# Kernel optimization log

Measured on AMD Instinct MI355X. Metric: run time of the kernel, lower is better.

Reference implementation:

```python
import jax, jax.numpy as jnp
import numpy as np

B, T, C = 8, 1024, 2048
N_HEAD = 16
HEAD = C // N_HEAD  # 128


def setup_inputs() -> dict:
    key = jax.random.key(0)
    k1, k2, k3 = jax.random.split(key, 3)
    scale = 0.02
    x = jax.random.normal(k1, (B, T, C), dtype=jnp.float32)
    W_attn = jax.random.normal(k2, (C, 3 * C), dtype=jnp.float32) * scale
    b_attn = jnp.zeros((3 * C,), dtype=jnp.float32)
    W_proj = jax.random.normal(k3, (C, C), dtype=jnp.float32) * scale
    b_proj = jnp.zeros((C,), dtype=jnp.float32)
    return {"x": x, "W_attn": W_attn, "b_attn": b_attn, "W_proj": W_proj, "b_proj": b_proj}


def reference(x, W_attn, b_attn, W_proj, b_proj):
    Bq, Tq, Cq = x.shape
    qkv = x @ W_attn + b_attn                       # [B,T,3C]
    q, k, v = jnp.split(qkv, 3, axis=2)             # each [B,T,C]
    def heads(t):
        return t.reshape(Bq, Tq, N_HEAD, HEAD).transpose(0, 2, 1, 3)  # [B,H,T,D]
    q, k, v = heads(q), heads(k), heads(v)
    scores = jnp.einsum('bhqd,bhkd->bhqk', q, k) / jnp.sqrt(jnp.float32(HEAD))
    causal = jnp.tril(jnp.ones((Tq, Tq), dtype=bool))
    scores = jnp.where(causal, scores, jnp.float32(-1e9))
    attn = jax.nn.softmax(scores, axis=-1)          # [B,H,T,T]
    y = jnp.einsum('bhqk,bhkd->bhqd', attn, v)      # [B,H,T,D]
    y = y.transpose(0, 2, 1, 3).reshape(Bq, Tq, Cq) # [B,T,C]
    return y @ W_proj + b_proj
```

## Files before the change

kernel.cpp:

```cpp
#include <hip/hip_runtime.h>
#include <hip/hip_bf16.h>


typedef unsigned short u16;
typedef __bf16 bf16x8 __attribute__((ext_vector_type(8)));
typedef float f32x4 __attribute__((ext_vector_type(4)));

#define B_ 8
#define T_ 1024
#define C_ 2048
#define NH 16
#define HD 128
#define BH (B_*NH)

__device__ __forceinline__ u16 f2b(float f){
  __bf16 h = (__bf16)f; return __builtin_bit_cast(u16, h);
}
__device__ __forceinline__ unsigned pk2(float x, float y){
  return (unsigned)f2b(x) | ((unsigned)f2b(y) << 16);
}
__device__ __forceinline__ bf16x8 ldfrag(const u16* p){
  uint4 u = *(const uint4*)p; return __builtin_bit_cast(bf16x8, u);
}
__device__ __forceinline__ void glds16(const u16* g, const u16* l){
  __builtin_amdgcn_global_load_lds(
      (const __attribute__((address_space(1))) void*)g,
      (__attribute__((address_space(3))) void*)l, 16, 0, 0);
}
__device__ __forceinline__ void sbar(){
  __builtin_amdgcn_sched_barrier(0);
  __builtin_amdgcn_s_barrier();
  __builtin_amdgcn_sched_barrier(0);
}

__global__ __launch_bounds__(256) void cvt_bf16(
    const float4* __restrict__ in, ushort4* __restrict__ outp, int n4)
{
  int i = blockIdx.x*256 + threadIdx.x;
  const int stride = gridDim.x*256;
  for (; i < n4; i += stride){
    float4 f = in[i];
    ushort4 o; o.x = f2b(f.x); o.y = f2b(f.y); o.z = f2b(f.z); o.w = f2b(f.w);
    outp[i] = o;
  }
}

__global__ __launch_bounds__(256) void transpose_cvt(
    const float* __restrict__ in, u16* __restrict__ outp, int R, int C)
{
  __shared__ u16 tile[64][65];
  const int t = threadIdx.x;
  const int r0 = blockIdx.y * 64, c0 = blockIdx.x * 64;
#pragma unroll
  for (int ii = 0; ii < 16; ++ii){
    int idx = t + ii*256; int r = idx >> 6, c = idx & 63;
    tile[r][c] = f2b(in[(size_t)(r0 + r)*C + c0 + c]);
  }
  __syncthreads();
#pragma unroll
  for (int ii = 0; ii < 16; ++ii){
    int idx = t + ii*256; int r = idx >> 6, c = idx & 63;
    outp[(size_t)(c0 + r)*R + r0 + c] = tile[c][r];
  }
}

__device__ __forceinline__ void qkv_epilogue(
    const f32x4 acc[4][4], const float* bias, int bx, int by,
    int wm, int wn, int lq, int ln,
    u16* qb, u16* kb, u16* vb)
{
  const int tensor = bx >> 4, h = bx & 15, b = by >> 3, t0 = (by & 7)*128;
  u16* tb = tensor==0 ? qb : (tensor==1 ? kb : vb);
  u16* op = tb + ((size_t)(b*NH + h)*T_ + t0)*HD;
#pragma unroll
  for (int j=0;j<4;j++){
    const float bv = bias[bx*128 + wn*64 + j*16 + ln];
    const int n = wn*64 + j*16 + ln;
#pragma unroll
    for (int i=0;i<4;i++){
      const int m0 = wm*64 + i*16 + lq*4;
#pragma unroll
      for (int r=0;r<4;r++)
        op[(size_t)(m0 + r)*HD + n] = f2b(acc[i][j][r] + bv);
    }
  }
}

__global__ __launch_bounds__(512,2) void gemm_qkv_8p(
    const u16* __restrict__ Xb, const u16* __restrict__ Wt,
    const float* __restrict__ bias,
    u16* __restrict__ qb, u16* __restrict__ kb, u16* __restrict__ vb)
{
  __shared__ u16 lds[2][2][256*64];
  const int t = threadIdx.x;
  const int lane = t & 63, wid = t >> 6;
  const int lq = lane >> 4, ln = lane & 15;
  const int wm = wid >> 2, wn = wid & 3;

  const int bid0 = blockIdx.x;
  const int bid = (bid0 & 7)*96 + (bid0 >> 3);
  const int bx = bid % 24, by = bid / 24;

  const int rl  = (wid << 4) + (lane >> 3);
  const int sw0 = (lane & 7) ^ (rl & 7);
  const int sw1 = (lane & 7) ^ ((rl + 8) & 7);
  const u16* Ag = Xb + ((size_t)(by*256) + rl)*2048;
  const u16* Bg = Wt + ((size_t)(bx*256) + rl)*2048;
  const size_t q0off = (size_t)sw0*8;
  const size_t q1off = (size_t)8*2048 + (size_t)sw1*8;

#define STAGE(buf_, op_, h_, T_) do { \
    const u16* s_ = (op_ ? Bg : Ag) + (size_t)(h_)*(128*2048) + (size_t)(T_)*64; \
    const u16* d_ = &lds[buf_][op_][(((h_)*128) + (wid<<4))*64]; \
    glds16(s_ + q0off, d_); \
    glds16(s_ + q1off, d_ + 8*64); \
  } while(0)

  const int swr0 = (0*4 + lq) ^ (ln & 7);
  const int swr1 = (1*4 + lq) ^ (ln & 7);

  const f32x4 fz = {0.f,0.f,0.f,0.f};
  f32x4 acc[8][4];
#pragma unroll
  for (int f=0;f<8;f++)
#pragma unroll
    for (int g=0;g<4;g++) acc[f][g] = fz;

  STAGE(0,0,0,0); STAGE(0,0,1,0); STAGE(0,1,0,0); STAGE(0,1,1,0);
  STAGE(1,1,0,1); STAGE(1,1,1,1); STAGE(1,0,0,1);
  asm volatile("s_waitcnt vmcnt(6)" ::: "memory");
  sbar();

  for (int T = 0; T < 32; ++T){
    const int b = T & 1;
    const u16* As = lds[b][0];
    const u16* Bs = lds[b][1];
    bf16x8 a0[4][2], a4[4][2], bfr[4][2];

#pragma unroll
    for (int f=0;f<4;f++){
      a0[f][0]  = ldfrag(&As[(wm*128 + f*16 + ln)*64 + swr0*8]);
      a0[f][1]  = ldfrag(&As[(wm*128 + f*16 + ln)*64 + swr1*8]);
      bfr[f][0] = ldfrag(&Bs[(wn*64  + f*16 + ln)*64 + swr0*8]);
      bfr[f][1] = ldfrag(&Bs[(wn*64  + f*16 + ln)*64 + swr1*8]);
    }
    if (T+1 < 32) STAGE(b^1, 0, 1, T+1);
    sbar();
    __builtin_amdgcn_s_setprio(1);
#pragma unroll
    for (int f=0;f<4;f++)
#pragma unroll
      for (int g=0;g<2;g++){
        acc[f][g] = __builtin_amdgcn_mfma_f32_16x16x32_bf16(a0[f][0], bfr[g][0], acc[f][g], 0,0,0);
        acc[f][g] = __builtin_amdgcn_mfma_f32_16x16x32_bf16(a0[f][1], bfr[g][1], acc[f][g], 0,0,0);
      }
    __builtin_amdgcn_s_setprio(0);
    sbar();

#pragma unroll
    for (int f=0;f<4;f++){
      a4[f][0] = ldfrag(&As[(wm*128 + (f+4)*16 + ln)*64 + swr0*8]);
      a4[f][1] = ldfrag(&As[(wm*128 + (f+4)*16 + ln)*64 + swr1*8]);
    }
    if (T+2 < 32) STAGE(b, 1, 0, T+2);
    sbar();
    __builtin_amdgcn_s_setprio(1);
#pragma unroll
    for (int f=0;f<4;f++)
#pragma unroll
      for (int g=0;g<2;g++){
        acc[f+4][g] = __builtin_amdgcn_mfma_f32_16x16x32_bf16(a4[f][0], bfr[g][0], acc[f+4][g], 0,0,0);
        acc[f+4][g] = __builtin_amdgcn_mfma_f32_16x16x32_bf16(a4[f][1], bfr[g][1], acc[f+4][g], 0,0,0);
      }
    __builtin_amdgcn_s_setprio(0);
    sbar();

    if (T+2 < 32) STAGE(b, 1, 1, T+2);
    sbar();
    __builtin_amdgcn_s_setprio(1);
#pragma unroll
    for (int f=0;f<4;f++)
#pragma unroll
      for (int g=2;g<4;g++){
        acc[f+4][g] = __builtin_amdgcn_mfma_f32_16x16x32_bf16(a4[f][0], bfr[g][0], acc[f+4][g], 0,0,0);
        acc[f+4][g] = __builtin_amdgcn_mfma_f32_16x16x32_bf16(a4[f][1], bfr[g][1], acc[f+4][g], 0,0,0);
      }
    __builtin_amdgcn_s_setprio(0);
    sbar();

    if (T+2 < 32) STAGE(b, 0, 0, T+2);
    if (T >= 30) asm volatile("s_waitcnt vmcnt(0)" ::: "memory");
    else         asm volatile("s_waitcnt vmcnt(6)" ::: "memory");
    sbar();
    __builtin_amdgcn_s_setprio(1);
#pragma unroll
    for (int f=0;f<4;f++)
#pragma unroll
      for (int g=2;g<4;g++){
        acc[f][g] = __builtin_amdgcn_mfma_f32_16x16x32_bf16(a0[f][0], bfr[g][0], acc[f][g], 0,0,0);
        acc[f][g] = __builtin_amdgcn_mfma_f32_16x16x32_bf16(a0[f][1], bfr[g][1], acc[f][g], 0,0,0);
      }
    __builtin_amdgcn_s_setprio(0);
    sbar();
  }
#undef STAGE

  const int tensor = bx >> 3;
  u16* tb = tensor==0 ? qb : (tensor==1 ? kb : vb);
  const int m_base = by*256 + wm*128;
#pragma unroll
  for (int g=0; g<4; ++g){
    const int ncol = (bx & 7)*256 + wn*64 + g*16 + ln;
    const float bv = bias[tensor*2048 + ncol];
    const int h = ncol >> 7, d = ncol & 127;
#pragma unroll
    for (int f=0; f<8; ++f){
      const int m0 = m_base + f*16 + lq*4;
      const int bb = m0 >> 10, tt = m0 & 1023;
      u16* op = tb + ((size_t)(bb*NH + h)*T_ + tt)*HD + d;
#pragma unroll
      for (int r=0;r<4;++r)
        op[(size_t)r*HD] = f2b(acc[f][g][r] + bv);
    }
  }
}

__global__ __launch_bounds__(256,2) void gemm_qkv_f32(
    const float* __restrict__ X, const u16* __restrict__ Wt, const float* __restrict__ bias,
    u16* __restrict__ qb, u16* __restrict__ kb, u16* __restrict__ vb)
{
  __shared__ u16 As[128*32];
  __shared__ u16 Bs[128*32];
  const int t = threadIdx.x;
  const int bx = blockIdx.x, by = blockIdx.y;
  const int lane = t & 63, wv = t >> 6;
  const int lq = lane >> 4, ln = lane & 15;
  const int wm = wv >> 1, wn = wv & 1;

  const int ar = t >> 1, ah = t & 1;
  const float* Ap = X + (size_t)(by*128 + ar)*2048 + ah*16;
  u16* AsW = &As[ar*32 + ah*16];

  const int c0 = t, c1 = 256 + t;
  const u16* Bp0 = Wt + (size_t)(bx*128 + (c0 >> 2))*2048 + (c0 & 3)*8;
  const u16* Bp1 = Wt + (size_t)(bx*128 + (c1 >> 2))*2048 + (c1 & 3)*8;
  const u16* BsW0 = &Bs[(wv*64)*8];
  const u16* BsW1 = &Bs[(256 + wv*64)*8];

  const f32x4 fz = {0.f,0.f,0.f,0.f};
  f32x4 acc[4][4];
#pragma unroll
  for (int i=0;i<4;i++)
#pragma unroll
    for (int j=0;j<4;j++) acc[i][j] = fz;

  for (int kt = 0; kt < 64; ++kt){
    float4 a0 = *(const float4*)(Ap);
    float4 a1 = *(const float4*)(Ap + 4);
    float4 a2 = *(const float4*)(Ap + 8);
    float4 a3 = *(const float4*)(Ap + 12);
    Ap += 32;
    __syncthreads();
    uint4 w0, w1;
    w0.x = pk2(a0.x,a0.y); w0.y = pk2(a0.z,a0.w);
    w0.z = pk2(a1.x,a1.y); w0.w = pk2(a1.z,a1.w);
    w1.x = pk2(a2.x,a2.y); w1.y = pk2(a2.z,a2.w);
    w1.z = pk2(a3.x,a3.y); w1.w = pk2(a3.z,a3.w);
    *(uint4*)(AsW) = w0; *(uint4*)(AsW + 8) = w1;
    glds16(Bp0, BsW0);
    glds16(Bp1, BsW1);
    Bp0 += 32; Bp1 += 32;
    __syncthreads();
    bf16x8 af[4], bf[4];
#pragma unroll
    for (int i=0;i<4;i++) af[i] = ldfrag(&As[(wm*64 + i*16 + ln)*32 + lq*8]);
#pragma unroll
    for (int j=0;j<4;j++) bf[j] = ldfrag(&Bs[(wn*64 + j*16 + ln)*32 + lq*8]);
#pragma unroll
    for (int i=0;i<4;i++)
#pragma unroll
      for (int j=0;j<4;j++)
        acc[i][j] = __builtin_amdgcn_mfma_f32_16x16x32_bf16(af[i], bf[j], acc[i][j], 0,0,0);
  }
  qkv_epilogue(acc, bias, bx, by, wm, wn, lq, ln, qb, kb, vb);
}

__global__ __launch_bounds__(256,2) void gemm_proj(
    const u16* __restrict__ Y, const u16* __restrict__ Wt, const float* __restrict__ bias,
    float* __restrict__ outp)
{
  __shared__ u16 As[128*32];
  __shared__ u16 Bs[128*32];
  const int t = threadIdx.x;
  const int bx = blockIdx.x, by = blockIdx.y;
  const int lane = t & 63, wv = t >> 6;
  const int lq = lane >> 4, ln = lane & 15;
  const int wm = wv >> 1, wn = wv & 1;

  const int c0 = t, c1 = 256 + t;
  const int rA0 = by*128 + (c0 >> 2), rA1 = by*128 + (c1 >> 2);
  const u16* Ya0 = Y + ((size_t)((rA0 >> 10)*NH)*T_ + (rA0 & 1023))*HD;
  const u16* Ya1 = Y + ((size_t)((rA1 >> 10)*NH)*T_ + (rA1 & 1023))*HD;
  const int kc0 = (c0 & 3)*8, kc1 = (c1 & 3)*8;
  const u16* AsW0 = &As[(wv*64)*8];
  const u16* AsW1 = &As[(256 + wv*64)*8];

  const u16* Bp0 = Wt + (size_t)(bx*128 + (c0 >> 2))*2048 + (c0 & 3)*8;
  const u16* Bp1 = Wt + (size_t)(bx*128 + (c1 >> 2))*2048 + (c1 & 3)*8;
  const u16* BsW0 = &Bs[(wv*64)*8];
  const u16* BsW1 = &Bs[(256 + wv*64)*8];

  const f32x4 fz = {0.f,0.f,0.f,0.f};
  f32x4 acc[4][4];
#pragma unroll
  for (int i=0;i<4;i++)
#pragma unroll
    for (int j=0;j<4;j++) acc[i][j] = fz;

  for (int kt = 0; kt < 64; ++kt){
    __syncthreads();
    {
      const int k0 = kt*32 + kc0, k1 = kt*32 + kc1;
      glds16(Ya0 + (size_t)(k0 >> 7)*(T_*HD) + (k0 & 127), AsW0);
      glds16(Ya1 + (size_t)(k1 >> 7)*(T_*HD) + (k1 & 127), AsW1);
      glds16(Bp0, BsW0);
      glds16(Bp1, BsW1);
      Bp0 += 32; Bp1 += 32;
    }
    __syncthreads();
    bf16x8 af[4], bf[4];
#pragma unroll
    for (int i=0;i<4;i++) af[i] = ldfrag(&As[(wm*64 + i*16 + ln)*32 + lq*8]);
#pragma unroll
    for (int j=0;j<4;j++) bf[j] = ldfrag(&Bs[(wn*64 + j*16 + ln)*32 + lq*8]);
#pragma unroll
    for (int i=0;i<4;i++)
#pragma unroll
      for (int j=0;j<4;j++)
        acc[i][j] = __builtin_amdgcn_mfma_f32_16x16x32_bf16(af[i], bf[j], acc[i][j], 0,0,0);
  }

  float* op = outp + (size_t)(by*128)*2048 + bx*128;
#pragma unroll
  for (int j=0;j<4;j++){
    const float bv = bias[bx*128 + wn*64 + j*16 + ln];
    const int n = wn*64 + j*16 + ln;
#pragma unroll
    for (int i=0;i<4;i++){
      const int m0 = wm*64 + i*16 + lq*4;
#pragma unroll
      for (int r=0;r<4;r++)
        op[(size_t)(m0 + r)*2048 + n] = acc[i][j][r] + bv;
    }
  }
}

__global__ __launch_bounds__(256,2) void attn_fwd(
    u16* qy, const u16* __restrict__ kk, const u16* __restrict__ vv)
{
  __shared__ u16 Ks[64*128];
  __shared__ u16 Vt[128*64];
  __shared__ u16 Ps[4*32*64];
  const int qt = 7 - blockIdx.x, bh = blockIdx.y;
  const int t = threadIdx.x;
  const int lane = t & 63, wv = t >> 6;
  const int lq = lane >> 4, ln = lane & 15;

  bf16x8 qf[2][4];
#pragma unroll
  for (int i=0;i<2;i++)
#pragma unroll
    for (int kc=0;kc<4;kc++){
      int qrow = qt*128 + wv*32 + i*16 + ln;
      qf[i][kc] = ldfrag(&qy[((size_t)bh*T_ + qrow)*HD + kc*32 + lq*8]);
    }

  const f32x4 fz = {0.f,0.f,0.f,0.f};
  f32x4 o[2][8];
#pragma unroll
  for (int i=0;i<2;i++)
#pragma unroll
    for (int jd=0;jd<8;jd++) o[i][jd] = fz;
  float mi[2][4], li[2][4];
#pragma unroll
  for (int i=0;i<2;i++)
#pragma unroll
    for (int r=0;r<4;r++){ mi[i][r] = -1e30f; li[i][r] = 0.f; }

  const float scale = 0.08838834764831843f;
  const int kr = t & 63, dbase = (t >> 6)*32;
  const int nkt = 2*qt + 2;

  uint4 kreg[4];
  uint4 vreg[4];
  {
    const uint4* ksrc = (const uint4*)(kk + (size_t)bh*T_*HD);
#pragma unroll
    for (int ii=0; ii<4; ++ii) kreg[ii] = ksrc[t + ii*256];
#pragma unroll
    for (int ch=0; ch<4; ++ch)
      vreg[ch] = *(const uint4*)&vv[((size_t)bh*T_ + kr)*HD + dbase + ch*8];
  }

  for (int kt = 0; kt < nkt; ++kt){
    __syncthreads();
    uint4* kdst = (uint4*)Ks;
#pragma unroll
    for (int ii=0; ii<4; ++ii){
      const int c = t + ii*256;
      kdst[(c & ~15) | ((c & 15) ^ ((c >> 4) & 7))] = kreg[ii];
    }
#pragma unroll
    for (int ch=0; ch<4; ++ch){
      const u16* e = (const u16*)&vreg[ch];
#pragma unroll
      for (int j=0; j<8; ++j){
        const int d = dbase + ch*8 + j;
        Vt[d*64 + (kr ^ ((d & 7) << 3))] = e[j];
      }
    }
    __syncthreads();

    {
      const int ktn = (kt+1 < nkt) ? kt+1 : kt;
      const uint4* ksrc = (const uint4*)(kk + ((size_t)bh*T_ + ktn*64)*HD);
#pragma unroll
      for (int ii=0; ii<4; ++ii) kreg[ii] = ksrc[t + ii*256];
#pragma unroll
      for (int ch=0; ch<4; ++ch)
        vreg[ch] = *(const uint4*)&vv[((size_t)bh*T_ + ktn*64 + kr)*HD + dbase + ch*8];
    }

    f32x4 s[2][4];
#pragma unroll
    for (int i=0;i<2;i++)
#pragma unroll
      for (int j=0;j<4;j++) s[i][j] = fz;
    __builtin_amdgcn_s_setprio(1);
#pragma unroll
    for (int j=0;j<4;j++){
      bf16x8 kf[4];
      const int krow = j*16 + ln;
      const int ksw = (krow & 7) << 3;
#pragma unroll
      for (int kc=0;kc<4;kc++)
        kf[kc] = ldfrag(&Ks[krow*128 + ((kc*32 + lq*8) ^ ksw)]);
#pragma unroll
      for (int i=0;i<2;i++)
#pragma unroll
        for (int kc=0;kc<4;kc++)
          s[i][j] = __builtin_amdgcn_mfma_f32_16x16x32_bf16(qf[i][kc], kf[kc], s[i][j], 0,0,0);
    }
    __builtin_amdgcn_s_setprio(0);

#pragma unroll
    for (int i=0;i<2;i++)
#pragma unroll
      for (int j=0;j<4;j++)
#pragma unroll
        for (int r=0;r<4;r++){
          int qg = qt*128 + wv*32 + i*16 + lq*4 + r;
          int kg = kt*64 + j*16 + ln;
          float sv = s[i][j][r]*scale;
          s[i][j][r] = (kg > qg) ? -1e30f : sv;
        }

    float mxv[2][4];
#pragma unroll
    for (int i=0;i<2;i++)
#pragma unroll
      for (int r=0;r<4;r++){
        float mx = fmaxf(fmaxf(s[i][0][r], s[i][1][r]), fmaxf(s[i][2][r], s[i][3][r]));
        mx = fmaxf(mx, __shfl_xor(mx, 1));
        mx = fmaxf(mx, __shfl_xor(mx, 2));
        mx = fmaxf(mx, __shfl_xor(mx, 4));
        mx = fmaxf(mx, __shfl_xor(mx, 8));
        mxv[i][r] = mx;
      }
    bool ok = true;
#pragma unroll
    for (int i=0;i<2;i++)
#pragma unroll
      for (int r=0;r<4;r++) ok = ok && (mxv[i][r] <= mi[i][r] + 8.0f);
    if (!__all((int)ok)){
#pragma unroll
      for (int i=0;i<2;i++)
#pragma unroll
        for (int r=0;r<4;r++){
          float mnew = fmaxf(mi[i][r], mxv[i][r]);
          float alpha = __expf(mi[i][r] - mnew);
          li[i][r] *= alpha;
          mi[i][r] = mnew;
#pragma unroll
          for (int jd=0;jd<8;jd++) o[i][jd][r] *= alpha;
        }
    }
#pragma unroll
    for (int i=0;i<2;i++)
#pragma unroll
      for (int r=0;r<4;r++){
        float rs = 0.f;
#pragma unroll
        for (int j=0;j<4;j++){
          float p = __expf(s[i][j][r] - mi[i][r]);
          s[i][j][r] = p; rs += p;
        }
        rs += __shfl_xor(rs, 1); rs += __shfl_xor(rs, 2);
        rs += __shfl_xor(rs, 4); rs += __shfl_xor(rs, 8);
        li[i][r] += rs;
      }

#pragma unroll
    for (int i=0;i<2;i++)
#pragma unroll
      for (int j=0;j<4;j++)
#pragma unroll
        for (int r=0;r<4;r++){
          const int rr = i*16 + lq*4 + r;
          Ps[wv*2048 + rr*64 + ((j*16 + ln) ^ ((rr & 7) << 3))] = f2b(s[i][j][r]);
        }

    bf16x8 pf[2][2];
#pragma unroll
    for (int i=0;i<2;i++){
      const int prow = i*16 + ln;
      const int psw = (prow & 7) << 3;
#pragma unroll
      for (int kc=0;kc<2;kc++)
        pf[i][kc] = ldfrag(&Ps[wv*2048 + prow*64 + ((kc*32 + lq*8) ^ psw)]);
    }
    __builtin_amdgcn_s_setprio(1);
#pragma unroll
    for (int jd=0;jd<8;jd++){
      const int vrow = jd*16 + ln;
      const int vsw = (vrow & 7) << 3;
#pragma unroll
      for (int kc=0;kc<2;kc++){
        bf16x8 vf = ldfrag(&Vt[vrow*64 + ((kc*32 + lq*8) ^ vsw)]);
#pragma unroll
        for (int i=0;i<2;i++)
          o[i][jd] = __builtin_amdgcn_mfma_f32_16x16x32_bf16(pf[i][kc], vf, o[i][jd], 0,0,0);
      }
    }
    __builtin_amdgcn_s_setprio(0);
  }

#pragma unroll
  for (int i=0;i<2;i++)
#pragma unroll
    for (int r=0;r<4;r++){
      float inv = 1.f / li[i][r];
      int row = qt*128 + wv*32 + i*16 + lq*4 + r;
#pragma unroll
      for (int jd=0;jd<8;jd++)
        qy[((size_t)bh*T_ + row)*HD + jd*16 + ln] = f2b(o[i][jd][r] * inv);
    }
}

extern "C" void kernel_launch(void* const* d_in, const int* in_sizes, int n_in,
                              void* d_out, int out_size, void* d_ws, size_t ws_size,
                              hipStream_t stream)
{
  const float* x      = (const float*)d_in[0];
  const float* W_attn = (const float*)d_in[1];
  const float* b_attn = (const float*)d_in[2];
  const float* W_proj = (const float*)d_in[3];
  const float* b_proj = (const float*)d_in[4];
  float* out = (float*)d_out;

  u16* Wat = (u16*)d_ws;
  u16* Wpt = Wat + (size_t)6144*2048;
  u16* qb  = Wpt + (size_t)2048*2048;
  u16* xb  = qb  + (size_t)BH*T_*HD;
  u16* kb  = (u16*)d_out;
  u16* vb  = kb + (size_t)BH*T_*HD;

  const size_t need = ((size_t)6144*2048 + (size_t)2048*2048
                       + 2*(size_t)BH*T_*HD) * sizeof(u16);

  hipLaunchKernelGGL(transpose_cvt, dim3(96,32,1), dim3(256,1,1), 0, stream,
                     W_attn, Wat, 2048, 6144);
  hipLaunchKernelGGL(transpose_cvt, dim3(32,32,1), dim3(256,1,1), 0, stream,
                     W_proj, Wpt, 2048, 2048);
  if (ws_size >= need){
    hipLaunchKernelGGL(cvt_bf16, dim3(1024,1,1), dim3(256,1,1), 0, stream,
                       (const float4*)x, (ushort4*)xb, (B_*T_*C_)/4);
    hipLaunchKernelGGL(gemm_qkv_8p, dim3(768,1,1), dim3(512,1,1), 0, stream,
                       xb, Wat, b_attn, qb, kb, vb);
  } else {
    hipLaunchKernelGGL(gemm_qkv_f32, dim3(48,64,1), dim3(256,1,1), 0, stream,
                       x, Wat, b_attn, qb, kb, vb);
  }
  hipLaunchKernelGGL(attn_fwd, dim3(8,BH,1), dim3(256,1,1), 0, stream,
                     qb, kb, vb);
  hipLaunchKernelGGL(gemm_proj, dim3(16,64,1), dim3(256,1,1), 0, stream,
                     qb, Wpt, b_proj, out);
}
```

Before: 627.8 us.

## Port projection GEMM to 8-phase pipelined kernel and skip fully-masked attention tiles

Replaces the simple 128x128 projection GEMM with a 256x256-tile, 512-thread, double-buffered, 8-phase pipelined kernel. It reads the head-major attention output directly through a per-row address mapping. In attention, each wave now skips the QK/softmax/PV work for key tiles that lie entirely above its causal diagonal. It also simplifies the QKV swizzle offset (sw1 equals sw0 because rl+8 has the same low 3 bits). The main risks are more register pressure and fewer blocks (256) for the projection, and wave divergence inside the attention block around barriers.

```diff
diff --git a/kernel.cpp b/kernel.cpp
--- a/kernel.cpp
+++ b/kernel.cpp
@@ -103,11 +103,10 @@
 
   const int rl  = (wid << 4) + (lane >> 3);
   const int sw0 = (lane & 7) ^ (rl & 7);
-  const int sw1 = (lane & 7) ^ ((rl + 8) & 7);
   const u16* Ag = Xb + ((size_t)(by*256) + rl)*2048;
   const u16* Bg = Wt + ((size_t)(bx*256) + rl)*2048;
   const size_t q0off = (size_t)sw0*8;
-  const size_t q1off = (size_t)8*2048 + (size_t)sw1*8;
+  const size_t q1off = (size_t)8*2048 + (size_t)sw0*8;
 
 #define STAGE(buf_, op_, h_, T_) do { \
     const u16* s_ = (op_ ? Bg : Ag) + (size_t)(h_)*(128*2048) + (size_t)(T_)*64; \
@@ -221,6 +220,145 @@
 #pragma unroll
       for (int r=0;r<4;++r)
         op[(size_t)r*HD] = f2b(acc[f][g][r] + bv);
+    }
+  }
+}
+
+__global__ __launch_bounds__(512,2) void gemm_proj_8p(
+    const u16* __restrict__ Y, const u16* __restrict__ Wt,
+    const float* __restrict__ bias, float* __restrict__ outp)
+{
+  __shared__ u16 lds[2][2][256*64];
+  const int t = threadIdx.x;
+  const int lane = t & 63, wid = t >> 6;
+  const int lq = lane >> 4, ln = lane & 15;
+  const int wm = wid >> 2, wn = wid & 3;
+
+  const int bid0 = blockIdx.x;
+  const int bid = (bid0 & 7)*32 + (bid0 >> 3);
+  const int bx = bid & 7, by = bid >> 3;
+
+  const int rl  = (wid << 4) + (lane >> 3);
+  const int sw0 = (lane & 7) ^ (rl & 7);
+  const u16* Bg = Wt + ((size_t)(bx*256) + rl)*2048;
+  const size_t bq0 = (size_t)sw0*8;
+  const size_t arow0 = ((size_t)(by >> 2)*16)*1024 + (size_t)(by & 3)*256 + rl;
+
+#define STAGEP(buf_, op_, h_, Tt_) do { \
+    const u16* d_ = &lds[buf_][op_][(((h_)*128) + (wid<<4))*64]; \
+    if (op_){ \
+      const u16* s_ = Bg + (size_t)(h_)*(128*2048) + (size_t)(Tt_)*64; \
+      glds16(s_ + bq0, d_); \
+      glds16(s_ + (size_t)8*2048 + bq0, d_ + 8*64); \
+    } else { \
+      const u16* s_ = Y + (arow0 + (size_t)((Tt_) >> 1)*1024 + (size_t)(h_)*128)*128 \
+                        + ((Tt_) & 1)*64 + sw0*8; \
+      glds16(s_, d_); \
+      glds16(s_ + 8*128, d_ + 8*64); \
+    } \
+  } while(0)
+
+  const int swr0 = (0*4 + lq) ^ (ln & 7);
+  const int swr1 = (1*4 + lq) ^ (ln & 7);
+
+  const f32x4 fz = {0.f,0.f,0.f,0.f};
+  f32x4 acc[8][4];
+#pragma unroll
+  for (int f=0;f<8;f++)
+#pragma unroll
+    for (int g=0;g<4;g++) acc[f][g] = fz;
+
+  STAGEP(0,0,0,0); STAGEP(0,0,1,0); STAGEP(0,1,0,0); STAGEP(0,1,1,0);
+  STAGEP(1,1,0,1); STAGEP(1,1,1,1); STAGEP(1,0,0,1);
+  asm volatile("s_waitcnt vmcnt(6)" ::: "memory");
+  sbar();
+
+  for (int T = 0; T < 32; ++T){
+    const int b = T & 1;
+    const u16* As = lds[b][0];
+    const u16* Bs = lds[b][1];
+    bf16x8 a0[4][2], a4[4][2], bfr[4][2];
+
+#pragma unroll
+    for (int f=0;f<4;f++){
+      a0[f][0]  = ldfrag(&As[(wm*128 + f*16 + ln)*64 + swr0*8]);
+      a0[f][1]  = ldfrag(&As[(wm*128 + f*16 + ln)*64 + swr1*8]);
+      bfr[f][0] = ldfrag(&Bs[(wn*64  + f*16 + ln)*64 + swr0*8]);
+      bfr[f][1] = ldfrag(&Bs[(wn*64  + f*16 + ln)*64 + swr1*8]);
+    }
+    if (T+1 < 32) STAGEP(b^1, 0, 1, T+1);
+    sbar();
+    __builtin_amdgcn_s_setprio(1);
+#pragma unroll
+    for (int f=0;f<4;f++)
+#pragma unroll
+      for (int g=0;g<2;g++){
+        acc[f][g] = __builtin_amdgcn_mfma_f32_16x16x32_bf16(a0[f][0], bfr[g][0], acc[f][g], 0,0,0);
+        acc[f][g] = __builtin_amdgcn_mfma_f32_16x16x32_bf16(a0[f][1], bfr[g][1], acc[f][g], 0,0,0);
+      }
+    __builtin_amdgcn_s_setprio(0);
+    sbar();
+
+#pragma unroll
+    for (int f=0;f<4;f++){
+      a4[f][0] = ldfrag(&As[(wm*128 + (f+4)*16 + ln)*64 + swr0*8]);
+      a4[f][1] = ldfrag(&As[(wm*128 + (f+4)*16 + ln)*64 + swr1*8]);
+    }
+    if (T+2 < 32) STAGEP(b, 1, 0, T+2);
+    sbar();
+    __builtin_amdgcn_s_setprio(1);
+#pragma unroll
+    for (int f=0;f<4;f++)
+#pragma unroll
+      for (int g=0;g<2;g++){
+        acc[f+4][g] = __builtin_amdgcn_mfma_f32_16x16x32_bf16(a4[f][0], bfr[g][0], acc[f+4][g], 0,0,0);
+        acc[f+4][g] = __builtin_amdgcn_mfma_f32_16x16x32_bf16(a4[f][1], bfr[g][1], acc[f+4][g], 0,0,0);
+      }
+    __builtin_amdgcn_s_setprio(0);
+    sbar();
+
+    if (T+2 < 32) STAGEP(b, 1, 1, T+2);
+    sbar();
+    __builtin_amdgcn_s_setprio(1);
+#pragma unroll
+    for (int f=0;f<4;f++)
+#pragma unroll
+      for (int g=2;g<4;g++){
+        acc[f+4][g] = __builtin_amdgcn_mfma_f32_16x16x32_bf16(a4[f][0], bfr[g][0], acc[f+4][g], 0,0,0);
+        acc[f+4][g] = __builtin_amdgcn_mfma_f32_16x16x32_bf16(a4[f][1], bfr[g][1], acc[f+4][g], 0,0,0);
+      }
+    __builtin_amdgcn_s_setprio(0);
+    sbar();
+
+    if (T+2 < 32) STAGEP(b, 0, 0, T+2);
+    if (T >= 30) asm volatile("s_waitcnt vmcnt(0)" ::: "memory");
+    else         asm volatile("s_waitcnt vmcnt(6)" ::: "memory");
+    sbar();
+    __builtin_amdgcn_s_setprio(1);
+#pragma unroll
+    for (int f=0;f<4;f++)
+#pragma unroll
+      for (int g=2;g<4;g++){
+        acc[f][g] = __builtin_amdgcn_mfma_f32_16x16x32_bf16(a0[f][0], bfr[g][0], acc[f][g], 0,0,0);
+        acc[f][g] = __builtin_amdgcn_mfma_f32_16x16x32_bf16(a0[f][1], bfr[g][1], acc[f][g], 0,0,0);
+      }
+    __builtin_amdgcn_s_setprio(0);
+    sbar();
+  }
+#undef STAGEP
+
+  const int m_base = by*256 + wm*128;
+#pragma unroll
+  for (int g=0; g<4; ++g){
+    const int ncol = bx*256 + wn*64 + g*16 + ln;
+    const float bv = bias[ncol];
+#pragma unroll
+    for (int f=0; f<8; ++f){
+      const int m0 = m_base + f*16 + lq*4;
+      float* op = outp + (size_t)m0*2048 + ncol;
+#pragma unroll
+      for (int r=0;r<4;++r)
+        op[(size_t)r*2048] = acc[f][g][r] + bv;
     }
   }
 }
@@ -285,76 +423,6 @@
   qkv_epilogue(acc, bias, bx, by, wm, wn, lq, ln, qb, kb, vb);
 }
 
-__global__ __launch_bounds__(256,2) void gemm_proj(
-    const u16* __restrict__ Y, const u16* __restrict__ Wt, const float* __restrict__ bias,
-    float* __restrict__ outp)
-{
-  __shared__ u16 As[128*32];
-  __shared__ u16 Bs[128*32];
-  const int t = threadIdx.x;
-  const int bx = blockIdx.x, by = blockIdx.y;
-  const int lane = t & 63, wv = t >> 6;
-  const int lq = lane >> 4, ln = lane & 15;
-  const int wm = wv >> 1, wn = wv & 1;
-
-  const int c0 = t, c1 = 256 + t;
-  const int rA0 = by*128 + (c0 >> 2), rA1 = by*128 + (c1 >> 2);
-  const u16* Ya0 = Y + ((size_t)((rA0 >> 10)*NH)*T_ + (rA0 & 1023))*HD;
-  const u16* Ya1 = Y + ((size_t)((rA1 >> 10)*NH)*T_ + (rA1 & 1023))*HD;
-  const int kc0 = (c0 & 3)*8, kc1 = (c1 & 3)*8;
-  const u16* AsW0 = &As[(wv*64)*8];
-  const u16* AsW1 = &As[(256 + wv*64)*8];
-
-  const u16* Bp0 = Wt + (size_t)(bx*128 + (c0 >> 2))*2048 + (c0 & 3)*8;
-  const u16* Bp1 = Wt + (size_t)(bx*128 + (c1 >> 2))*2048 + (c1 & 3)*8;
-  const u16* BsW0 = &Bs[(wv*64)*8];
-  const u16* BsW1 = &Bs[(256 + wv*64)*8];
-
-  const f32x4 fz = {0.f,0.f,0.f,0.f};
-  f32x4 acc[4][4];
-#pragma unroll
-  for (int i=0;i<4;i++)
-#pragma unroll
-    for (int j=0;j<4;j++) acc[i][j] = fz;
-
-  for (int kt = 0; kt < 64; ++kt){
-    __syncthreads();
-    {
-      const int k0 = kt*32 + kc0, k1 = kt*32 + kc1;
-      glds16(Ya0 + (size_t)(k0 >> 7)*(T_*HD) + (k0 & 127), AsW0);
-      glds16(Ya1 + (size_t)(k1 >> 7)*(T_*HD) + (k1 & 127), AsW1);
-      glds16(Bp0, BsW0);
-      glds16(Bp1, BsW1);
-      Bp0 += 32; Bp1 += 32;
-    }
-    __syncthreads();
-    bf16x8 af[4], bf[4];
-#pragma unroll
-    for (int i=0;i<4;i++) af[i] = ldfrag(&As[(wm*64 + i*16 + ln)*32 + lq*8]);
-#pragma unroll
-    for (int j=0;j<4;j++) bf[j] = ldfrag(&Bs[(wn*64 + j*16 + ln)*32 + lq*8]);
-#pragma unroll
-    for (int i=0;i<4;i++)
-#pragma unroll
-      for (int j=0;j<4;j++)
-        acc[i][j] = __builtin_amdgcn_mfma_f32_16x16x32_bf16(af[i], bf[j], acc[i][j], 0,0,0);
-  }
-
-  float* op = outp + (size_t)(by*128)*2048 + bx*128;
-#pragma unroll
-  for (int j=0;j<4;j++){
-    const float bv = bias[bx*128 + wn*64 + j*16 + ln];
-    const int n = wn*64 + j*16 + ln;
-#pragma unroll
-    for (int i=0;i<4;i++){
-      const int m0 = wm*64 + i*16 + lq*4;
-#pragma unroll
-      for (int r=0;r<4;r++)
-        op[(size_t)(m0 + r)*2048 + n] = acc[i][j][r] + bv;
-    }
-  }
-}
-
 __global__ __launch_bounds__(256,2) void attn_fwd(
     u16* qy, const u16* __restrict__ kk, const u16* __restrict__ vv)
 {
@@ -431,6 +499,9 @@
         vreg[ch] = *(const uint4*)&vv[((size_t)bh*T_ + ktn*64 + kr)*HD + dbase + ch*8];
     }
 
+    const bool active = (kt*64) <= (qt*128 + wv*32 + 31);
+    if (active){
+
     f32x4 s[2][4];
 #pragma unroll
     for (int i=0;i<2;i++)
@@ -543,6 +614,8 @@
       }
     }
     __builtin_amdgcn_s_setprio(0);
+
+    }
   }
 
 #pragma unroll
@@ -593,6 +666,6 @@
   }
   hipLaunchKernelGGL(attn_fwd, dim3(8,BH,1), dim3(256,1,1), 0, stream,
                      qb, kb, vb);
-  hipLaunchKernelGGL(gemm_proj, dim3(16,64,1), dim3(256,1,1), 0, stream,
+  hipLaunchKernelGGL(gemm_proj_8p, dim3(256,1,1), dim3(512,1,1), 0, stream,
                      qb, Wpt, b_proj, out);
 }
```

Measured after the change: 605.7 us. -3.5%, faster.
